# Kernel tuning notes

Measured on AMD Instinct MI355X. Metric: run time of the kernel, lower is better.

The kernel has to match this reference:

```python
import jax, jax.numpy as jnp
import numpy as np

B, N, D, H = 128, 512, 128, 8
DH = D // H
CLIP = 10.0          # tanh_clipping
NEG = -1.0e9         # finite -inf for masking (keeps grads clean)


def setup_inputs() -> dict:
    key = jax.random.key(0)
    ks = jax.random.split(key, 6)
    s = 0.08  # ~1/sqrt(D) init scale so pre-tanh logits are in a sane range
    return {
        "embeddings": jax.random.normal(ks[0], (B, N, D), jnp.float32),
        "W_node_proj": jax.random.normal(ks[1], (D, 3 * D), jnp.float32) * s,
        "W_fixed_ctx": jax.random.normal(ks[2], (D, D), jnp.float32) * s,
        "W_step_ctx": jax.random.normal(ks[3], (2 * D, D), jnp.float32) * s,
        "W_out": jax.random.normal(ks[4], (D, D), jnp.float32) * s,
        "W_placeholder": jax.random.uniform(ks[5], (2 * D,), jnp.float32, -1.0, 1.0),
    }


def reference(embeddings, W_node_proj, W_fixed_ctx, W_step_ctx, W_out, W_placeholder):
    # _precompute: fixed context + glimpse K/V + logit key (cached for all steps)
    graph_embed = embeddings.mean(axis=1)                    # [B,D]
    fixed_ctx = graph_embed @ W_fixed_ctx                    # [B,D]
    proj = embeddings @ W_node_proj                          # [B,N,3D]
    gK, gV, logit_K = jnp.split(proj, 3, axis=-1)
    gK = gK.reshape(B, N, H, DH)                             # glimpse key heads
    gV = gV.reshape(B, N, H, DH)                             # glimpse val heads
    inv_sqrt_dh = 1.0 / jnp.sqrt(jnp.float32(DH))
    inv_sqrt_d = 1.0 / jnp.sqrt(jnp.float32(D))
    batch_idx = jnp.arange(B)

    def step(carry, _):
        visited, first, prev, i = carry
        # step context: placeholder at i==0, else concat(first, current) embeddings
        cur_ctx = jnp.concatenate(
            [embeddings[batch_idx, first], embeddings[batch_idx, prev]], axis=-1)  # [B,2D]
        step_ctx = jnp.where(i == 0, W_placeholder[None, :], cur_ctx)
        q = fixed_ctx + step_ctx @ W_step_ctx                # [B,D]
        qh = q.reshape(B, H, DH)
        # masked multi-head glimpse attention
        compat = jnp.einsum('bhd,bnhd->bhn', qh, gK) * inv_sqrt_dh
        compat = jnp.where(visited[:, None, :], NEG, compat)
        attn = jax.nn.softmax(compat, axis=-1)
        heads = jnp.einsum('bhn,bnhd->bhd', attn, gV)
        glimpse = heads.reshape(B, D) @ W_out                # project_out
        # logit attention with tanh clipping
        logits = jnp.einsum('bd,bnd->bn', glimpse, logit_K) * inv_sqrt_d
        logits = CLIP * jnp.tanh(logits)
        logits = jnp.where(visited, NEG, logits)
        log_p = jax.nn.log_softmax(logits, axis=-1)
        sel = jnp.argmax(log_p, axis=-1).astype(jnp.int32)   # greedy decode
        visited = visited.at[batch_idx, sel].set(True)
        first = jnp.where(i == 0, sel, first)
        return (visited, first, sel, i + 1), (log_p, sel)

    init = (jnp.zeros((B, N), bool), jnp.zeros((B,), jnp.int32),
            jnp.zeros((B,), jnp.int32), jnp.int32(0))
    _, (log_ps, pis) = jax.lax.scan(step, init, None, length=N)
    log_p = jnp.transpose(log_ps, (1, 0, 2))                 # [B,N_steps,N]
    pi = jnp.transpose(pis, (1, 0))                          # [B,N_steps]
    # _calc_log_likelihood
    ll = jnp.take_along_axis(log_p, pi[:, :, None], axis=2).squeeze(-1).sum(axis=1)
    return log_p, pi, ll
```

## Files before the change

kernel.cpp:

```cpp
#include <hip/hip_runtime.h>
#include <hip/hip_bf16.h>
#include <math.h>

#define BATCH 128
#define NN 512
#define DD 128
#define D3 384
#define NEGV (-1.0e9f)
#define NEGINF (-1.0e30f)

__global__ __launch_bounds__(256) void k_fixed(const float* __restrict__ emb,
                                               const float* __restrict__ Wf,
                                               const float* __restrict__ Wstep,
                                               const float* __restrict__ Wph,
                                               float* __restrict__ fixedc,
                                               float* __restrict__ q0) {
  const int b = blockIdx.x;
  __shared__ float s_part[2][DD];
  __shared__ float s_ge[DD];
  const int tid = threadIdx.x;
  const int d = tid & 127, c = tid >> 7;
  const float* e = emb + (size_t)b * NN * DD;
  float acc = 0.f;
  for (int n = c * 256; n < c * 256 + 256; ++n) acc += e[(size_t)n * DD + d];
  s_part[c][d] = acc;
  __syncthreads();
  if (tid < DD) s_ge[tid] = (s_part[0][tid] + s_part[1][tid]) * (1.0f / 512.0f);
  __syncthreads();
  if (tid < DD) {
    float a = 0.f;
    for (int k = 0; k < DD; ++k) a += s_ge[k] * Wf[k * DD + tid];
    fixedc[b * DD + tid] = a;
    float pq = 0.f;
    for (int k = 0; k < 2 * DD; ++k) pq += Wph[k] * Wstep[k * DD + tid];
    q0[b * DD + tid] = a + pq;
  }
}

__global__ __launch_bounds__(384) void k_proj(const float* __restrict__ emb,
                                              const float* __restrict__ Wp,
                                              float* __restrict__ proj) {
  const size_t row0 = (size_t)blockIdx.x * 32;
  __shared__ float s_A[32][DD];
  const int tid = threadIdx.x;
  for (int t = tid; t < 32 * DD; t += 384)
    s_A[t >> 7][t & 127] = emb[row0 * DD + t];
  __syncthreads();
  float acc[32];
#pragma unroll
  for (int r = 0; r < 32; ++r) acc[r] = 0.f;
  const int c = tid;
  for (int k = 0; k < DD; ++k) {
    float w = Wp[k * D3 + c];
#pragma unroll
    for (int r = 0; r < 32; ++r) acc[r] += s_A[r][k] * w;
  }
  for (int r = 0; r < 32; ++r) proj[(row0 + r) * D3 + c] = acc[r];
}

__global__ __launch_bounds__(128) void k_lp(float* __restrict__ proj,
                                            const float* __restrict__ Wout) {
  const size_t row0 = (size_t)blockIdx.x * 32;
  __shared__ float s_L[32][DD];
  const int tid = threadIdx.x;
  for (int rr = 0; rr < 32; ++rr)
    s_L[rr][tid] = proj[(row0 + rr) * D3 + 2 * DD + tid];
  __syncthreads();
  float acc[32];
#pragma unroll
  for (int r = 0; r < 32; ++r) acc[r] = 0.f;
  for (int d = 0; d < DD; ++d) {
    const float w = Wout[tid * DD + d];
#pragma unroll
    for (int r = 0; r < 32; ++r) acc[r] += w * s_L[r][d];
  }
  for (int r = 0; r < 32; ++r)
    proj[(row0 + r) * D3 + 2 * DD + tid] = acc[r];
}

__global__ __launch_bounds__(256) void k_ectx(const float* __restrict__ emb,
                                              const float* __restrict__ Wstep,
                                              float* __restrict__ E12) {
  const size_t row0 = (size_t)blockIdx.x * 32;
  __shared__ float s_A[32][DD];
  const int tid = threadIdx.x;
  for (int t = tid; t < 32 * DD; t += 256)
    s_A[t >> 7][t & 127] = emb[row0 * DD + t];
  __syncthreads();
  float acc[32];
#pragma unroll
  for (int r = 0; r < 32; ++r) acc[r] = 0.f;
  const int c = tid;
  const float* wp = (c < DD) ? (Wstep + c) : (Wstep + DD * DD + (c - DD));
  for (int k = 0; k < DD; ++k) {
    float w = wp[(size_t)k * DD];
#pragma unroll
    for (int r = 0; r < 32; ++r) acc[r] += s_A[r][k] * w;
  }
  for (int r = 0; r < 32; ++r) E12[(row0 + r) * 256 + c] = acc[r];
}

__global__ __launch_bounds__(1024, 1) void k_decode(
    const float* __restrict__ emb, const float* __restrict__ proj,
    const float* __restrict__ fixedc, const float* __restrict__ q0,
    const float* __restrict__ E12, const float* __restrict__ Wstep,
    const float* __restrict__ Wph, const int useE, float* __restrict__ out) {
  const int b = blockIdx.x;
  const int tid = threadIdx.x;
  const int lane = tid & 63;
  const int wave = tid >> 6;
  const int h = tid & 7, r = tid >> 3;

  __shared__ int s_idx[NN];
  __shared__ int s_pos[NN];
  __shared__ unsigned char s_visited[NN];
  __shared__ float s_red[16][8];
  __shared__ float s_hacc[16][8][17];
  __shared__ float s_heads[DD];
  __shared__ float s_logits[NN];
  __shared__ float s_rm[16];
  __shared__ int s_ri[16];
  __shared__ float s_es[16];
  __shared__ float s_q[DD];
  __shared__ float s_ctx[2 * DD];
  __shared__ int s_first, s_prev, s_M;
  __shared__ float s_ll;

  const float inv_sqrt_d = 0.08838834764831845f;
  const size_t eb = (size_t)b * NN * DD;
  const size_t e2 = (size_t)b * NN * 256;
  const float* projb = proj + (size_t)b * NN * D3;
  float* outp = out + (size_t)b * NN * NN;
  const size_t PI_OFF = (size_t)BATCH * NN * NN;
  const size_t LL_OFF = PI_OFF + (size_t)BATCH * NN;

  float f16[16];
#pragma unroll
  for (int d = 0; d < 4; ++d) {
    const float4 v = *(const float4*)(fixedc + b * DD + h * 16 + d * 4);
    f16[d * 4 + 0] = v.x; f16[d * 4 + 1] = v.y;
    f16[d * 4 + 2] = v.z; f16[d * 4 + 3] = v.w;
  }

  if (tid < NN) {
    s_idx[tid] = tid;
    s_pos[tid] = tid;
    s_visited[tid] = 0;
  }
  if (tid == 0) { s_first = 0; s_prev = 0; s_ll = 0.f; s_M = NN; }
  __syncthreads();

  for (int i = 0; i < NN; ++i) {
    const int M = s_M;
    const int first = s_first, prev = s_prev;

    float qf[16];
    if (useE) {
      if (i == 0) {
#pragma unroll
        for (int d = 0; d < 4; ++d) {
          const float4 v = *(const float4*)(q0 + b * DD + h * 16 + d * 4);
          qf[d * 4 + 0] = v.x; qf[d * 4 + 1] = v.y;
          qf[d * 4 + 2] = v.z; qf[d * 4 + 3] = v.w;
        }
      } else {
        const float* e1p = E12 + e2 + (size_t)first * 256 + h * 16;
        const float* e2p = E12 + e2 + (size_t)prev * 256 + DD + h * 16;
#pragma unroll
        for (int d = 0; d < 4; ++d) {
          const float4 a = *(const float4*)(e1p + d * 4);
          const float4 c = *(const float4*)(e2p + d * 4);
          qf[d * 4 + 0] = f16[d * 4 + 0] + a.x + c.x;
          qf[d * 4 + 1] = f16[d * 4 + 1] + a.y + c.y;
          qf[d * 4 + 2] = f16[d * 4 + 2] + a.z + c.z;
          qf[d * 4 + 3] = f16[d * 4 + 3] + a.w + c.w;
        }
      }
    } else {
      if (tid < 2 * DD) {
        float v;
        if (i == 0)
          v = Wph[tid];
        else
          v = (tid < DD) ? emb[eb + (size_t)first * DD + tid]
                         : emb[eb + (size_t)prev * DD + (tid - DD)];
        s_ctx[tid] = v;
      }
      __syncthreads();
      if (tid < DD) {
        float a = (tid < DD) ? fixedc[b * DD + tid] : 0.f;
        for (int k = 0; k < 2 * DD; ++k) a += s_ctx[k] * Wstep[k * DD + tid];
        s_q[tid] = a;
      }
      __syncthreads();
#pragma unroll
      for (int d = 0; d < 16; ++d) qf[d] = s_q[h * 16 + d];
    }

    bool act[4];
    int nj[4];
#pragma unroll
    for (int k = 0; k < 4; ++k) {
      const int j = r + k * 128;
      act[k] = (j < M);
      nj[k] = s_idx[j];
    }
    float cc[4];
    float mloc = NEGINF;
#pragma unroll
    for (int k = 0; k < 4; ++k) {
      float cv = NEGINF;
      if (act[k]) {
        const float4* kp =
            (const float4*)(projb + (size_t)nj[k] * D3 + h * 16);
        float4 k0 = kp[0], k1 = kp[1], k2 = kp[2], k3 = kp[3];
        float a = qf[0] * k0.x + qf[1] * k0.y + qf[2] * k0.z + qf[3] * k0.w +
                  qf[4] * k1.x + qf[5] * k1.y + qf[6] * k1.z + qf[7] * k1.w +
                  qf[8] * k2.x + qf[9] * k2.y + qf[10] * k2.z + qf[11] * k2.w +
                  qf[12] * k3.x + qf[13] * k3.y + qf[14] * k3.z +
                  qf[15] * k3.w;
        cv = a * 0.25f;
      }
      cc[k] = cv;
      mloc = fmaxf(mloc, cv);
    }
#pragma unroll
    for (int off = 8; off <= 32; off <<= 1)
      mloc = fmaxf(mloc, __shfl_xor(mloc, off));
    if (lane < 8) s_red[wave][lane] = mloc;
    if (tid >= 512) {
      const int t2 = tid - 512;
      if (s_visited[t2]) s_logits[t2] = NEGV;
    }
    __syncthreads();

    float mh = NEGINF;
#pragma unroll
    for (int w = 0; w < 16; ++w) mh = fmaxf(mh, s_red[w][h]);
    float ssum = 0.f;
    float acc[16];
#pragma unroll
    for (int d = 0; d < 16; ++d) acc[d] = 0.f;
#pragma unroll
    for (int k = 0; k < 4; ++k) {
      if (act[k]) {
        const float p = expf(cc[k] - mh);
        ssum += p;
        const float4* vp =
            (const float4*)(projb + (size_t)nj[k] * D3 + DD + h * 16);
        float4 v0 = vp[0], v1 = vp[1], v2 = vp[2], v3 = vp[3];
        acc[0] += p * v0.x;  acc[1] += p * v0.y;
        acc[2] += p * v0.z;  acc[3] += p * v0.w;
        acc[4] += p * v1.x;  acc[5] += p * v1.y;
        acc[6] += p * v1.z;  acc[7] += p * v1.w;
        acc[8] += p * v2.x;  acc[9] += p * v2.y;
        acc[10] += p * v2.z; acc[11] += p * v2.w;
        acc[12] += p * v3.x; acc[13] += p * v3.y;
        acc[14] += p * v3.z; acc[15] += p * v3.w;
      }
    }
#pragma unroll
    for (int off = 8; off <= 32; off <<= 1) {
      ssum += __shfl_xor(ssum, off);
#pragma unroll
      for (int d = 0; d < 16; ++d) acc[d] += __shfl_xor(acc[d], off);
    }
    if (lane < 8) {
      s_hacc[wave][lane][16] = ssum;
#pragma unroll
      for (int d = 0; d < 16; ++d) s_hacc[wave][lane][d] = acc[d];
    }
    __syncthreads();

    if (tid < DD) {
      const int hh = tid >> 4, dh = tid & 15;
      float a = 0.f, s = 0.f;
#pragma unroll
      for (int w = 0; w < 16; ++w) {
        a += s_hacc[w][hh][dh];
        s += s_hacc[w][hh][16];
      }
      s_heads[tid] = a / s;
    }
    __syncthreads();

    float gf[16];
#pragma unroll
    for (int d = 0; d < 16; ++d) gf[d] = s_heads[h * 16 + d];
    float av = NEGINF;
    int ai = 0x7FFFFFFF;
    float asum = 0.f;
#pragma unroll
    for (int k = 0; k < 4; ++k) {
      if (act[k]) {
        const float4* lp =
            (const float4*)(projb + (size_t)nj[k] * D3 + 2 * DD + h * 16);
        float4 l0 = lp[0], l1 = lp[1], l2 = lp[2], l3 = lp[3];
        float a = gf[0] * l0.x + gf[1] * l0.y + gf[2] * l0.z + gf[3] * l0.w +
                  gf[4] * l1.x + gf[5] * l1.y + gf[6] * l1.z + gf[7] * l1.w +
                  gf[8] * l2.x + gf[9] * l2.y + gf[10] * l2.z + gf[11] * l2.w +
                  gf[12] * l3.x + gf[13] * l3.y + gf[14] * l3.z +
                  gf[15] * l3.w;
        a += __shfl_xor(a, 1);
        a += __shfl_xor(a, 2);
        a += __shfl_xor(a, 4);
        if (h == 0) {
          const float lg = 10.0f * tanhf(a * inv_sqrt_d);
          s_logits[nj[k]] = lg;
          asum += expf(lg);
          if (lg > av || (lg == av && nj[k] < ai)) { av = lg; ai = nj[k]; }
        }
      }
    }
#pragma unroll
    for (int off = 1; off <= 32; off <<= 1) {
      const float ov = __shfl_xor(av, off);
      const int oi = __shfl_xor(ai, off);
      asum += __shfl_xor(asum, off);
      if (ov > av || (ov == av && oi < ai)) { av = ov; ai = oi; }
    }
    if (lane == 0) { s_rm[wave] = av; s_ri[wave] = ai; s_es[wave] = asum; }
    __syncthreads();

    float bv = s_rm[0];
    int bi = s_ri[0];
    float bs = s_es[0];
#pragma unroll
    for (int w2 = 1; w2 < 16; ++w2) {
      const float ov = s_rm[w2];
      const int oi = s_ri[w2];
      bs += s_es[w2];
      if (ov > bv || (ov == bv && oi < bi)) { bv = ov; bi = oi; }
    }
    const float lz = logf(bs);
    const int sel = bi;
    if (tid < NN) outp[(size_t)i * NN + tid] = s_logits[tid] - lz;
    if (tid == 0) {
      s_ll += s_logits[sel] - lz;
      s_visited[sel] = 1;
      if (i == 0) s_first = sel;
      s_prev = sel;
      out[PI_OFF + (size_t)b * NN + i] = (float)sel;
      const int p = s_pos[sel];
      const int last = s_idx[M - 1];
      s_idx[p] = last;
      s_pos[last] = p;
      s_idx[M - 1] = sel;
      s_pos[sel] = M - 1;
      s_M = M - 1;
    }
    __syncthreads();
  }
  if (tid == 0) out[LL_OFF + b] = s_ll;
}

extern "C" void kernel_launch(void* const* d_in, const int* in_sizes, int n_in,
                              void* d_out, int out_size, void* d_ws,
                              size_t ws_size, hipStream_t stream) {
  const float* emb = (const float*)d_in[0];
  const float* Wnp = (const float*)d_in[1];
  const float* Wf = (const float*)d_in[2];
  const float* Wstep = (const float*)d_in[3];
  const float* Wout = (const float*)d_in[4];
  const float* Wph = (const float*)d_in[5];
  float* out = (float*)d_out;

  const size_t projN = (size_t)BATCH * NN * D3;
  const size_t eN = (size_t)BATCH * NN * 256;
  const size_t need_full = (projN + eN + 2 * (size_t)BATCH * DD) * 4;

  float* proj = (float*)d_ws;
  float* E12 = proj + projN;
  const int useE = (ws_size >= need_full) ? 1 : 0;
  float* fixedc = useE ? (E12 + eN) : (proj + projN);
  float* q0 = fixedc + (size_t)BATCH * DD;

  k_fixed<<<BATCH, 256, 0, stream>>>(emb, Wf, Wstep, Wph, fixedc, q0);
  k_proj<<<(BATCH * NN) / 32, 384, 0, stream>>>(emb, Wnp, proj);
  k_lp<<<(BATCH * NN) / 32, 128, 0, stream>>>(proj, Wout);
  if (useE) k_ectx<<<(BATCH * NN) / 32, 256, 0, stream>>>(emb, Wstep, E12);
  k_decode<<<BATCH, 1024, 0, stream>>>(emb, proj, fixedc, q0,
                                       useE ? E12 : nullptr, Wstep, Wph, useE,
                                       out);
}
```

Baseline: 7.042 ms.

## Use per-wave online softmax in glimpse to drop a block barrier

Replaces the block-wide max reduction and its barrier with per-lane local maxima. The partial sums are rescaled with the wave max, and a final cross-wave merge in shared memory applies exp weights. The reduction of the 16-wide accumulator across lanes now uses a recursive-halving shuffle exchange, so each lane sends one value per dimension pair instead of 16 full butterfly shuffles. Key loads are also issued before the dot products to overlap memory latency. This removes one __syncthreads per decode step and cuts shuffle traffic, at the cost of extra expf calls and more registers.

```diff
diff --git a/kernel.cpp b/kernel.cpp
--- a/kernel.cpp
+++ b/kernel.cpp
@@ -188,7 +188,7 @@
       }
       __syncthreads();
       if (tid < DD) {
-        float a = (tid < DD) ? fixedc[b * DD + tid] : 0.f;
+        float a = fixedc[b * DD + tid];
         for (int k = 0; k < 2 * DD; ++k) a += s_ctx[k] * Wstep[k * DD + tid];
         s_q[tid] = a;
       }
@@ -205,47 +205,43 @@
       act[k] = (j < M);
       nj[k] = s_idx[j];
     }
+    float4 Kf[4][4];
+#pragma unroll
+    for (int k = 0; k < 4; ++k) {
+      if (act[k]) {
+        const float4* kp = (const float4*)(projb + (size_t)nj[k] * D3 + h * 16);
+        Kf[k][0] = kp[0]; Kf[k][1] = kp[1];
+        Kf[k][2] = kp[2]; Kf[k][3] = kp[3];
+      }
+    }
     float cc[4];
-    float mloc = NEGINF;
+    float m_l = NEGINF;
 #pragma unroll
     for (int k = 0; k < 4; ++k) {
       float cv = NEGINF;
       if (act[k]) {
-        const float4* kp =
-            (const float4*)(projb + (size_t)nj[k] * D3 + h * 16);
-        float4 k0 = kp[0], k1 = kp[1], k2 = kp[2], k3 = kp[3];
-        float a = qf[0] * k0.x + qf[1] * k0.y + qf[2] * k0.z + qf[3] * k0.w +
-                  qf[4] * k1.x + qf[5] * k1.y + qf[6] * k1.z + qf[7] * k1.w +
-                  qf[8] * k2.x + qf[9] * k2.y + qf[10] * k2.z + qf[11] * k2.w +
-                  qf[12] * k3.x + qf[13] * k3.y + qf[14] * k3.z +
-                  qf[15] * k3.w;
+        float a = qf[0] * Kf[k][0].x + qf[1] * Kf[k][0].y +
+                  qf[2] * Kf[k][0].z + qf[3] * Kf[k][0].w +
+                  qf[4] * Kf[k][1].x + qf[5] * Kf[k][1].y +
+                  qf[6] * Kf[k][1].z + qf[7] * Kf[k][1].w +
+                  qf[8] * Kf[k][2].x + qf[9] * Kf[k][2].y +
+                  qf[10] * Kf[k][2].z + qf[11] * Kf[k][2].w +
+                  qf[12] * Kf[k][3].x + qf[13] * Kf[k][3].y +
+                  qf[14] * Kf[k][3].z + qf[15] * Kf[k][3].w;
         cv = a * 0.25f;
       }
       cc[k] = cv;
-      mloc = fmaxf(mloc, cv);
-    }
-#pragma unroll
-    for (int off = 8; off <= 32; off <<= 1)
-      mloc = fmaxf(mloc, __shfl_xor(mloc, off));
-    if (lane < 8) s_red[wave][lane] = mloc;
-    if (tid >= 512) {
-      const int t2 = tid - 512;
-      if (s_visited[t2]) s_logits[t2] = NEGV;
-    }
-    __syncthreads();
-
-    float mh = NEGINF;
-#pragma unroll
-    for (int w = 0; w < 16; ++w) mh = fmaxf(mh, s_red[w][h]);
-    float ssum = 0.f;
+      m_l = fmaxf(m_l, cv);
+    }
+    float s_l = 0.f;
     float acc[16];
 #pragma unroll
     for (int d = 0; d < 16; ++d) acc[d] = 0.f;
 #pragma unroll
     for (int k = 0; k < 4; ++k) {
       if (act[k]) {
-        const float p = expf(cc[k] - mh);
-        ssum += p;
+        const float p = expf(cc[k] - m_l);
+        s_l += p;
         const float4* vp =
             (const float4*)(projb + (size_t)nj[k] * D3 + DD + h * 16);
         float4 v0 = vp[0], v1 = vp[1], v2 = vp[2], v3 = vp[3];
@@ -259,28 +255,66 @@
         acc[14] += p * v3.z; acc[15] += p * v3.w;
       }
     }
-#pragma unroll
-    for (int off = 8; off <= 32; off <<= 1) {
-      ssum += __shfl_xor(ssum, off);
-#pragma unroll
-      for (int d = 0; d < 16; ++d) acc[d] += __shfl_xor(acc[d], off);
-    }
-    if (lane < 8) {
-      s_hacc[wave][lane][16] = ssum;
-#pragma unroll
-      for (int d = 0; d < 16; ++d) s_hacc[wave][lane][d] = acc[d];
-    }
+    float m8 = m_l;
+    m8 = fmaxf(m8, __shfl_xor(m8, 8));
+    m8 = fmaxf(m8, __shfl_xor(m8, 16));
+    m8 = fmaxf(m8, __shfl_xor(m8, 32));
+    const float sc = expf(m_l - m8);
+    s_l *= sc;
+#pragma unroll
+    for (int d = 0; d < 16; ++d) acc[d] *= sc;
+    s_l += __shfl_xor(s_l, 8);
+    s_l += __shfl_xor(s_l, 16);
+    s_l += __shfl_xor(s_l, 32);
+    {
+      const bool k1 = (lane & 8) == 0;
+#pragma unroll
+      for (int d = 0; d < 8; ++d) {
+        const float send = k1 ? acc[d + 8] : acc[d];
+        const float got = __shfl_xor(send, 8);
+        acc[d] = (k1 ? acc[d] : acc[d + 8]) + got;
+      }
+      const bool k2 = (lane & 16) == 0;
+#pragma unroll
+      for (int d = 0; d < 4; ++d) {
+        const float send = k2 ? acc[d + 4] : acc[d];
+        const float got = __shfl_xor(send, 16);
+        acc[d] = (k2 ? acc[d] : acc[d + 4]) + got;
+      }
+      const bool k3 = (lane & 32) == 0;
+#pragma unroll
+      for (int d = 0; d < 2; ++d) {
+        const float send = k3 ? acc[d + 2] : acc[d];
+        const float got = __shfl_xor(send, 32);
+        acc[d] = (k3 ? acc[d] : acc[d + 2]) + got;
+      }
+    }
+    {
+      const int dim0 = ((lane & 8) ? 8 : 0) | ((lane & 16) ? 4 : 0) |
+                       ((lane & 32) ? 2 : 0);
+      s_hacc[wave][h][dim0] = acc[0];
+      s_hacc[wave][h][dim0 + 1] = acc[1];
+      if (lane < 8) {
+        s_hacc[wave][lane][16] = s_l;
+        s_red[wave][lane] = m8;
+      }
+    }
+    if (tid < NN && s_visited[tid]) s_logits[tid] = NEGV;
     __syncthreads();
 
     if (tid < DD) {
       const int hh = tid >> 4, dh = tid & 15;
-      float a = 0.f, s = 0.f;
+      float m_g = NEGINF;
+#pragma unroll
+      for (int w = 0; w < 16; ++w) m_g = fmaxf(m_g, s_red[w][hh]);
+      float num = 0.f, den = 0.f;
 #pragma unroll
       for (int w = 0; w < 16; ++w) {
-        a += s_hacc[w][hh][dh];
-        s += s_hacc[w][hh][16];
-      }
-      s_heads[tid] = a / s;
+        const float wgt = expf(s_red[w][hh] - m_g);
+        num += wgt * s_hacc[w][hh][dh];
+        den += wgt * s_hacc[w][hh][16];
+      }
+      s_heads[tid] = num / den;
     }
     __syncthreads();
 
```

New measurement: 8.560 ms. 1.22x slower.
